# Performance work log

Measured on AMD Instinct MI355X. Metric: run time of the kernel, lower is better.

The kernel has to match this reference:

```python
import jax, jax.numpy as jnp
import numpy as np

N, E, D, L, G = 100000, 800000, 64, 5, 256
ATOM_VOCAB, BOND_VOCAB = 119, 5
BN_EPS = 1e-5

def _bn(h, g, b):
    # BatchNorm1d in training mode: batch mean / biased var over nodes
    m = h.mean(0)
    v = h.var(0)
    return g * (h - m) * jax.lax.rsqrt(v + BN_EPS) + b

def setup_inputs() -> dict:
    key = jax.random.key(0)
    ks = jax.random.split(key, 12)
    xavier = lambda k, fi, fo: jax.random.uniform(k, (fi, fo), jnp.float32,
                                                  -np.sqrt(6.0/(fi+fo)), np.sqrt(6.0/(fi+fo)))
    return {
        "batch": jnp.sort(jax.random.randint(ks[0], (N,), 0, G)),
        "x": jax.random.randint(ks[1], (N, 1), 0, ATOM_VOCAB),
        "edge_index": jax.random.randint(ks[2], (2, E), 0, N),
        "edge_attr": jax.random.randint(ks[3], (E, 1), 0, BOND_VOCAB),
        "atom_emb": jax.random.normal(ks[4], (ATOM_VOCAB, D), jnp.float32),
        "bond_emb": jax.random.normal(ks[5], (BOND_VOCAB, D), jnp.float32),
        "W1": jnp.stack([xavier(jax.random.fold_in(ks[6], i), D, 2*D) for i in range(L)]),
        "b1": jnp.zeros((L, 2*D), jnp.float32),
        "g1": jnp.ones((L, 2*D), jnp.float32),
        "be1": jnp.zeros((L, 2*D), jnp.float32),
        "W2": jnp.stack([xavier(jax.random.fold_in(ks[7], i), 2*D, D) for i in range(L)]),
        "b2": jnp.zeros((L, D), jnp.float32),
        "gbn": jnp.ones((L, D), jnp.float32),
        "bbn": jnp.zeros((L, D), jnp.float32),
    }

def reference(batch, x, edge_index, edge_attr, atom_emb, bond_emb,
              W1, b1, g1, be1, W2, b2, gbn, bbn):
    h = atom_emb[x[:, 0]]              # [N, D]
    ea = bond_emb[edge_attr[:, 0]]     # [E, D]
    src, dst = edge_index[0], edge_index[1]
    for i in range(L):
        msg = jax.nn.relu(h[src] + ea)                         # [E, D]
        aggr = jax.ops.segment_sum(msg, dst, num_segments=N)   # [N, D]
        z = h + aggr                                           # (1+eps)*x_i + aggr, eps=0
        z = _bn(z @ W1[i] + b1[i], g1[i], be1[i])
        z = jax.nn.relu(z) @ W2[i] + b2[i]
        h = _bn(z, gbn[i], bbn[i])                             # outer BN
        if i < L - 1:
            h = jax.nn.relu(h)                                 # drop_ratio = 0 -> no dropout
    xpool = jax.ops.segment_sum(h, batch, num_segments=G)      # global_add_pool
    return (xpool, h)
```

## Files before the change

kernel.cpp:

```cpp
#include <hip/hip_runtime.h>
#include <cstdint>
#include <cstddef>

#define NN 100000
#define NP 100032
#define NE 800000
#define NG 256
#define NL 5
#define EPS 1e-5f
#define NSTRIPE 32

typedef __bf16 bf16x8 __attribute__((ext_vector_type(8)));
typedef float f32x4 __attribute__((ext_vector_type(4)));

__device__ __forceinline__ float bf2f(unsigned short u) {
  union { unsigned int i; float f; } x; x.i = ((unsigned int)u) << 16; return x.f;
}
__device__ __forceinline__ unsigned short f2bf(float f) {
  union { float f; unsigned int i; } x; x.f = f;
  unsigned int r = x.i + 0x7fffu + ((x.i >> 16) & 1u);
  return (unsigned short)(r >> 16);
}

__global__ __launch_bounds__(256) void prep_k(const int* __restrict__ x,
                                              const float* __restrict__ atom_emb,
                                              unsigned short* __restrict__ A,
                                              const float* __restrict__ W1,
                                              const float* __restrict__ W2,
                                              unsigned short* __restrict__ Wt1,
                                              unsigned short* __restrict__ Wt2,
                                              int* __restrict__ cnt) {
  int b = blockIdx.x, t = threadIdx.x;
  if (b < 3125) {
    int i = b * 256 + t;
    int n = i >> 3, c0 = (i & 7) * 8;
    const float* p = atom_emb + (size_t)x[n] * 64 + c0;
    float4 v0 = *(const float4*)p;
    float4 v1 = *(const float4*)(p + 4);
    union { bf16x8 b8; unsigned short u[8]; } o;
    o.u[0] = f2bf(v0.x); o.u[1] = f2bf(v0.y); o.u[2] = f2bf(v0.z); o.u[3] = f2bf(v0.w);
    o.u[4] = f2bf(v1.x); o.u[5] = f2bf(v1.y); o.u[6] = f2bf(v1.z); o.u[7] = f2bf(v1.w);
    *(bf16x8*)(A + (size_t)n * 64 + c0) = o.b8;
  } else if (b < 3445) {
    int i = (b - 3125) * 256 + t;
    const int S = NL * 128 * 64;
    if (i < S) {
      int l = i / (128 * 64), r = i % (128 * 64);
      int c = r / 64, k = r % 64;
      Wt1[i] = f2bf(W1[(size_t)l * 64 * 128 + (size_t)k * 128 + c]);
    } else {
      int j = i - S;
      int l = j / (128 * 64), r = j % (128 * 64);
      int c = r / 128, k = r % 128;
      Wt2[j] = f2bf(W2[(size_t)l * 128 * 64 + (size_t)k * 64 + c]);
    }
  } else {
    int i = (b - 3445) * 256 + t;
    if (i < NN) cnt[i] = 0;
  }
}

__global__ __launch_bounds__(256) void hist_k(const int* __restrict__ ei,
                                              int* __restrict__ cnt) {
  int e = blockIdx.x * 256 + threadIdx.x;
  if (e >= NE) return;
  atomicAdd(&cnt[ei[NE + e]], 1);
}

__global__ __launch_bounds__(256) void scan1_k(const int* __restrict__ cnt,
                                               int* __restrict__ rs,
                                               int* __restrict__ bsum) {
  __shared__ int sh[256];
  int t = threadIdx.x;
  int base = blockIdx.x * 1024 + t * 4;
  int v0 = 0, v1 = 0, v2 = 0, v3 = 0;
  if (base + 0 < NN) v0 = cnt[base + 0];
  if (base + 1 < NN) v1 = cnt[base + 1];
  if (base + 2 < NN) v2 = cnt[base + 2];
  if (base + 3 < NN) v3 = cnt[base + 3];
  int tsum = v0 + v1 + v2 + v3;
  sh[t] = tsum;
  __syncthreads();
  for (int off = 1; off < 256; off <<= 1) {
    int x = (t >= off) ? sh[t - off] : 0;
    __syncthreads();
    sh[t] += x;
    __syncthreads();
  }
  int excl = sh[t] - tsum;
  if (base + 0 < NN) rs[base + 0] = excl;
  if (base + 1 < NN) rs[base + 1] = excl + v0;
  if (base + 2 < NN) rs[base + 2] = excl + v0 + v1;
  if (base + 3 < NN) rs[base + 3] = excl + v0 + v1 + v2;
  if (t == 255) bsum[blockIdx.x] = sh[255];
}

__global__ __launch_bounds__(256) void scan3_k(int* __restrict__ rs,
                                               const int* __restrict__ bsum,
                                               int* __restrict__ cursor) {
  int i = blockIdx.x * 256 + threadIdx.x;
  int chunk = blockIdx.x >> 2;
  int boff = 0;
  for (int j = 0; j < chunk; ++j) boff += bsum[j];
  if (i < NN) {
    int v = rs[i] + boff;
    rs[i] = v;
    cursor[i] = v;
  }
  if (i == 0) rs[NN] = NE;
}

__global__ __launch_bounds__(256) void scatter_k(const int* __restrict__ ei,
                                                 const int* __restrict__ eattr,
                                                 int* __restrict__ cursor,
                                                 int* __restrict__ epack) {
  int band = blockIdx.x & 3;
  int e = (blockIdx.x >> 2) * 256 + threadIdx.x;
  if (e >= NE) return;
  int d = ei[NE + e];
  if (d / 25000 != band) return;
  int slot = atomicAdd(&cursor[d], 1);
  epack[slot] = (ei[e] << 3) | eattr[e];
}

template <int MODE>
__global__ __launch_bounds__(256) void csr_aggr_k(const int* __restrict__ rowstart,
                                                  const int* __restrict__ epack,
                                                  const float* __restrict__ bond,
                                                  const unsigned short* __restrict__ A,
                                                  const float* __restrict__ stat2prev,
                                                  const float* __restrict__ g,
                                                  const float* __restrict__ be,
                                                  const unsigned short* __restrict__ Wt1,
                                                  unsigned short* __restrict__ B,
                                                  float* __restrict__ stat1) {
  __shared__ float bl[5][68];
  __shared__ float scl64[64], shf64[64];
  __shared__ unsigned short Bs[32][72];
  int tid = threadIdx.x;
  for (int j = tid; j < 320; j += 256) bl[j >> 6][j & 63] = bond[j];
  if (MODE && tid < 64) {
    float s = 0.f, s2 = 0.f;
#pragma unroll
    for (int r = 0; r < NSTRIPE; ++r) {
      s += stat2prev[r * 128 + tid];
      s2 += stat2prev[r * 128 + 64 + tid];
    }
    float mean = s * (1.f / NN);
    float var = fmaxf(s2 * (1.f / NN) - mean * mean, 0.f);
    float sc = g[tid] * rsqrtf(var + EPS);
    scl64[tid] = sc;
    shf64[tid] = be[tid] - mean * sc;
  }
  __syncthreads();

  int lane = tid & 63;
  int sg = lane >> 3, ch = lane & 7, c0 = ch * 8;
  int rloc = (tid >> 6) * 8 + sg;
  int row = blockIdx.x * 32 + rloc;
  float sc[8], sf[8];
  if (MODE) {
#pragma unroll
    for (int j = 0; j < 8; ++j) { sc[j] = scl64[c0 + j]; sf[j] = shf64[c0 + j]; }
  }
  int s = rowstart[row], e = rowstart[row + 1];
  float acc[8];
#pragma unroll
  for (int j = 0; j < 8; ++j) acc[j] = 0.f;
  int i = s;
  for (; i + 4 <= e; i += 4) {
    int p0 = epack[i], p1 = epack[i + 1], p2 = epack[i + 2], p3 = epack[i + 3];
    union { bf16x8 b; unsigned short u[8]; } h0, h1, h2, h3;
    h0.b = *(const bf16x8*)(A + (size_t)(p0 >> 3) * 64 + c0);
    h1.b = *(const bf16x8*)(A + (size_t)(p1 >> 3) * 64 + c0);
    h2.b = *(const bf16x8*)(A + (size_t)(p2 >> 3) * 64 + c0);
    h3.b = *(const bf16x8*)(A + (size_t)(p3 >> 3) * 64 + c0);
    const float* bp0 = &bl[p0 & 7][c0];
    const float* bp1 = &bl[p1 & 7][c0];
    const float* bp2 = &bl[p2 & 7][c0];
    const float* bp3 = &bl[p3 & 7][c0];
    float4 x0 = *(const float4*)(bp0), x1 = *(const float4*)(bp0 + 4);
    float4 y0 = *(const float4*)(bp1), y1 = *(const float4*)(bp1 + 4);
    float4 z0 = *(const float4*)(bp2), z1 = *(const float4*)(bp2 + 4);
    float4 w0 = *(const float4*)(bp3), w1 = *(const float4*)(bp3 + 4);
    float b0[8] = {x0.x, x0.y, x0.z, x0.w, x1.x, x1.y, x1.z, x1.w};
    float b1[8] = {y0.x, y0.y, y0.z, y0.w, y1.x, y1.y, y1.z, y1.w};
    float b2v[8] = {z0.x, z0.y, z0.z, z0.w, z1.x, z1.y, z1.z, z1.w};
    float b3[8] = {w0.x, w0.y, w0.z, w0.w, w1.x, w1.y, w1.z, w1.w};
#pragma unroll
    for (int j = 0; j < 8; ++j) {
      float v0 = bf2f(h0.u[j]);
      float v1 = bf2f(h1.u[j]);
      float v2 = bf2f(h2.u[j]);
      float v3 = bf2f(h3.u[j]);
      if (MODE) {
        v0 = fmaxf(fmaf(v0, sc[j], sf[j]), 0.f);
        v1 = fmaxf(fmaf(v1, sc[j], sf[j]), 0.f);
        v2 = fmaxf(fmaf(v2, sc[j], sf[j]), 0.f);
        v3 = fmaxf(fmaf(v3, sc[j], sf[j]), 0.f);
      }
      acc[j] += fmaxf(v0 + b0[j], 0.f);
      acc[j] += fmaxf(v1 + b1[j], 0.f);
      acc[j] += fmaxf(v2 + b2v[j], 0.f);
      acc[j] += fmaxf(v3 + b3[j], 0.f);
    }
  }
  for (; i < e; ++i) {
    int p0 = epack[i];
    union { bf16x8 b; unsigned short u[8]; } h0;
    h0.b = *(const bf16x8*)(A + (size_t)(p0 >> 3) * 64 + c0);
    const float* bp0 = &bl[p0 & 7][c0];
    float4 x0 = *(const float4*)(bp0), x1 = *(const float4*)(bp0 + 4);
    float b0[8] = {x0.x, x0.y, x0.z, x0.w, x1.x, x1.y, x1.z, x1.w};
#pragma unroll
    for (int j = 0; j < 8; ++j) {
      float v0 = bf2f(h0.u[j]);
      if (MODE) v0 = fmaxf(fmaf(v0, sc[j], sf[j]), 0.f);
      acc[j] += fmaxf(v0 + b0[j], 0.f);
    }
  }
  union { bf16x8 b; unsigned short u[8]; } rv, o;
  rv.b = *(const bf16x8*)(A + (size_t)row * 64 + c0);
#pragma unroll
  for (int j = 0; j < 8; ++j) {
    float r = bf2f(rv.u[j]);
    if (MODE) r = fmaxf(fmaf(r, sc[j], sf[j]), 0.f);
    o.u[j] = f2bf(acc[j] + r);
  }
  *(bf16x8*)(B + (size_t)row * 64 + c0) = o.b;
  *(bf16x8*)&Bs[rloc][c0] = o.b;
  __syncthreads();

  int w = tid >> 6;
  int rlo = lane & 15, khi = lane >> 4;
  int tile = w >> 1, gcol = (w & 1) * 64;
  bf16x8 fa0 = *(const bf16x8*)&Bs[tile * 16 + rlo][khi * 8];
  bf16x8 fa1 = *(const bf16x8*)&Bs[tile * 16 + rlo][khi * 8 + 32];
  float* dst = stat1 + (blockIdx.x & (NSTRIPE - 1)) * 256;
#pragma unroll
  for (int ct = 0; ct < 4; ++ct) {
    int c = gcol + ct * 16 + rlo;
    const bf16x8* bp = (const bf16x8*)(Wt1 + (size_t)c * 64 + khi * 8);
    f32x4 yacc;
    yacc[0] = 0.f; yacc[1] = 0.f; yacc[2] = 0.f; yacc[3] = 0.f;
    yacc = __builtin_amdgcn_mfma_f32_16x16x32_bf16(fa0, bp[0], yacc, 0, 0, 0);
    yacc = __builtin_amdgcn_mfma_f32_16x16x32_bf16(fa1, bp[4], yacc, 0, 0, 0);
    float ss = 0.f, ss2 = 0.f;
#pragma unroll
    for (int q = 0; q < 4; ++q) {
      ss += yacc[q];
      ss2 = fmaf(yacc[q], yacc[q], ss2);
    }
    ss += __shfl_xor(ss, 16);  ss += __shfl_xor(ss, 32);
    ss2 += __shfl_xor(ss2, 16); ss2 += __shfl_xor(ss2, 32);
    if (khi == 0) {
      atomicAdd(&dst[c], ss);
      atomicAdd(&dst[128 + c], ss2);
    }
  }
}

__global__ __launch_bounds__(256) void gemm12_k(const unsigned short* __restrict__ B,
                                                const unsigned short* __restrict__ Wt1,
                                                const unsigned short* __restrict__ Wt2,
                                                const float* __restrict__ stat1,
                                                const float* __restrict__ g1,
                                                const float* __restrict__ be1,
                                                const float* __restrict__ b2,
                                                unsigned short* __restrict__ z2b,
                                                float* __restrict__ stat2f) {
  __shared__ unsigned short Zs[64][136];
  __shared__ float sclS[128], shfS[128], sred[128];
  int tid = threadIdx.x;
  int w = tid >> 6, lane = tid & 63;
  int rlo = lane & 15, khi = lane >> 4;
  int row0 = blockIdx.x * 64 + w * 16;
  const bf16x8* ap = (const bf16x8*)(B + (size_t)(row0 + rlo) * 64 + khi * 8);
  bf16x8 a0 = ap[0], a1 = ap[4];
  if (tid < 128) {
    float s = 0.f, s2 = 0.f;
#pragma unroll
    for (int r = 0; r < NSTRIPE; ++r) {
      s += stat1[r * 256 + tid];
      s2 += stat1[r * 256 + 128 + tid];
    }
    float mean = s * (1.f / NN);
    float var = fmaxf(s2 * (1.f / NN) - mean * mean, 0.f);
    float sc = g1[tid] * rsqrtf(var + EPS);
    sclS[tid] = sc;
    shfS[tid] = be1[tid] - mean * sc;
    sred[tid] = 0.f;
  }
  __syncthreads();
#pragma unroll
  for (int ct = 0; ct < 8; ++ct) {
    const bf16x8* bp = (const bf16x8*)(Wt1 + (size_t)(ct * 16 + rlo) * 64 + khi * 8);
    f32x4 acc;
    acc[0] = 0.f; acc[1] = 0.f; acc[2] = 0.f; acc[3] = 0.f;
    acc = __builtin_amdgcn_mfma_f32_16x16x32_bf16(a0, bp[0], acc, 0, 0, 0);
    acc = __builtin_amdgcn_mfma_f32_16x16x32_bf16(a1, bp[4], acc, 0, 0, 0);
    int c = ct * 16 + rlo;
    float sc = sclS[c], sf = shfS[c];
#pragma unroll
    for (int q = 0; q < 4; ++q)
      Zs[w * 16 + khi * 4 + q][c] = f2bf(fmaxf(fmaf(acc[q], sc, sf), 0.f));
  }
  bf16x8 af0 = *(const bf16x8*)&Zs[w * 16 + rlo][khi * 8];
  bf16x8 af1 = *(const bf16x8*)&Zs[w * 16 + rlo][32 + khi * 8];
  bf16x8 af2 = *(const bf16x8*)&Zs[w * 16 + rlo][64 + khi * 8];
  bf16x8 af3 = *(const bf16x8*)&Zs[w * 16 + rlo][96 + khi * 8];
  __syncthreads();
  f32x4 acc2[4];
#pragma unroll
  for (int ct = 0; ct < 4; ++ct) { acc2[ct][0] = 0.f; acc2[ct][1] = 0.f; acc2[ct][2] = 0.f; acc2[ct][3] = 0.f; }
#pragma unroll
  for (int ct = 0; ct < 4; ++ct) {
    const bf16x8* bp = (const bf16x8*)(Wt2 + (size_t)(ct * 16 + rlo) * 128 + khi * 8);
    acc2[ct] = __builtin_amdgcn_mfma_f32_16x16x32_bf16(af0, bp[0], acc2[ct], 0, 0, 0);
    acc2[ct] = __builtin_amdgcn_mfma_f32_16x16x32_bf16(af1, bp[4], acc2[ct], 0, 0, 0);
    acc2[ct] = __builtin_amdgcn_mfma_f32_16x16x32_bf16(af2, bp[8], acc2[ct], 0, 0, 0);
    acc2[ct] = __builtin_amdgcn_mfma_f32_16x16x32_bf16(af3, bp[12], acc2[ct], 0, 0, 0);
  }
  unsigned short (*Z2)[72] = (unsigned short(*)[72])Zs;
#pragma unroll
  for (int ct = 0; ct < 4; ++ct) {
    int c = ct * 16 + rlo;
    float bs = b2[c];
    float s = 0.f, s2 = 0.f;
#pragma unroll
    for (int q = 0; q < 4; ++q) {
      int brow = w * 16 + khi * 4 + q;
      float v = acc2[ct][q] + bs;
      unsigned short ub = f2bf(v);
      Z2[brow][c] = ub;
      float vf = bf2f(ub);
      if (blockIdx.x * 64 + brow < NN) { s += vf; s2 += vf * vf; }
    }
    s += __shfl_xor(s, 16);  s += __shfl_xor(s, 32);
    s2 += __shfl_xor(s2, 16); s2 += __shfl_xor(s2, 32);
    if (khi == 0) {
      atomicAdd(&sred[c], s);
      atomicAdd(&sred[64 + c], s2);
    }
  }
  __syncthreads();
#pragma unroll
  for (int pass = 0; pass < 2; ++pass) {
    int orow = pass * 32 + (tid >> 3), oc0 = (tid & 7) * 8;
    *(bf16x8*)(z2b + (size_t)(blockIdx.x * 64 + orow) * 64 + oc0) =
        *(const bf16x8*)&Z2[orow][oc0];
  }
  if (tid < 128)
    atomicAdd(&stat2f[(blockIdx.x & (NSTRIPE - 1)) * 128 + tid], sred[tid]);
}

__global__ __launch_bounds__(256) void final_k(const unsigned short* __restrict__ A,
                                               const float* __restrict__ stat2f,
                                               const float* __restrict__ g,
                                               const float* __restrict__ be,
                                               const int* __restrict__ batch,
                                               float* __restrict__ hf,
                                               float* __restrict__ xpool) {
  __shared__ float scl[64], shf[64];
  __shared__ float red[16][64];
  __shared__ int gfirst, gsame;
  int tid = threadIdx.x;
  if (tid < 64) {
    float s = 0.f, s2 = 0.f;
#pragma unroll
    for (int r = 0; r < NSTRIPE; ++r) {
      s += stat2f[r * 128 + tid];
      s2 += stat2f[r * 128 + 64 + tid];
    }
    float mean = s * (1.f / NN);
    float var = fmaxf(s2 * (1.f / NN) - mean * mean, 0.f);
    float sc = g[tid] * rsqrtf(var + EPS);
    scl[tid] = sc;
    shf[tid] = be[tid] - mean * sc;
  }
  int n0 = blockIdx.x * 16;
  if (tid == 0) {
    gfirst = batch[n0];
    gsame = (batch[n0] == batch[n0 + 15]) ? 1 : 0;
  }
  __syncthreads();
  int r = tid >> 4, c4 = tid & 15;
  int n = n0 + r;
  ushort4 raw = *(const ushort4*)(A + (size_t)n * 64 + c4 * 4);
  int cb = c4 * 4;
  float4 v;
  v.x = fmaf(bf2f(raw.x), scl[cb + 0], shf[cb + 0]);
  v.y = fmaf(bf2f(raw.y), scl[cb + 1], shf[cb + 1]);
  v.z = fmaf(bf2f(raw.z), scl[cb + 2], shf[cb + 2]);
  v.w = fmaf(bf2f(raw.w), scl[cb + 3], shf[cb + 3]);
  *(float4*)(hf + (size_t)n * 64 + cb) = v;
  *(float4*)&red[r][cb] = v;
  __syncthreads();
  if (gsame) {
#pragma unroll
    for (int off = 8; off >= 1; off >>= 1) {
      if (r < off) {
        float4 a = *(float4*)&red[r][cb];
        float4 b = *(float4*)&red[r + off][cb];
        *(float4*)&red[r][cb] = make_float4(a.x + b.x, a.y + b.y, a.z + b.z, a.w + b.w);
      }
      __syncthreads();
    }
    if (r == 0) {
      float* p = xpool + (size_t)gfirst * 64 + cb;
      float4 a = *(float4*)&red[0][cb];
      atomicAdd(p + 0, a.x); atomicAdd(p + 1, a.y);
      atomicAdd(p + 2, a.z); atomicAdd(p + 3, a.w);
    }
  } else {
    int gg = batch[n];
    float* p = xpool + (size_t)gg * 64 + cb;
    atomicAdd(p + 0, v.x); atomicAdd(p + 1, v.y);
    atomicAdd(p + 2, v.z); atomicAdd(p + 3, v.w);
  }
}

extern "C" void kernel_launch(void* const* d_in, const int* in_sizes, int n_in,
                              void* d_out, int out_size, void* d_ws, size_t ws_size,
                              hipStream_t stream) {
  const int* batch = (const int*)d_in[0];
  const int* x = (const int*)d_in[1];
  const int* ei = (const int*)d_in[2];
  const int* eattr = (const int*)d_in[3];
  const float* atom_emb = (const float*)d_in[4];
  const float* bond_emb = (const float*)d_in[5];
  const float* W1 = (const float*)d_in[6];
  const float* g1 = (const float*)d_in[8];
  const float* be1 = (const float*)d_in[9];
  const float* W2 = (const float*)d_in[10];
  const float* b2 = (const float*)d_in[11];
  const float* gbn = (const float*)d_in[12];
  const float* bbn = (const float*)d_in[13];

  float* out = (float*)d_out;
  float* xpool = out;
  float* hf = out + NG * 64;

  char* ws = (char*)d_ws;
  unsigned short* A   = (unsigned short*)(ws);
  unsigned short* B   = (unsigned short*)(ws + 12804096);
  float* sbuf         = (float*)(ws + 25608192);
  unsigned short* Wt1 = (unsigned short*)(ws + 25853952);
  unsigned short* Wt2 = (unsigned short*)(ws + 25935872);
  int* rowstart       = (int*)(ws + 26017792);
  int* epack          = (int*)(ws + 26417796);
  int* cnt    = (int*)(ws + 12804096);
  int* cursor = (int*)(ws + 12804096 + 1048576);
  int* bsum   = (int*)(ws + 12804096 + 2097152);

  prep_k<<<3836, 256, 0, stream>>>(x, atom_emb, A, W1, W2, Wt1, Wt2, cnt);

  hist_k<<<(NE + 255) / 256, 256, 0, stream>>>(ei, cnt);
  scan1_k<<<98, 256, 0, stream>>>(cnt, rowstart, bsum);
  scan3_k<<<(NN + 255) / 256, 256, 0, stream>>>(rowstart, bsum, cursor);
  scatter_k<<<4 * ((NE + 255) / 256), 256, 0, stream>>>(ei, eattr, cursor, epack);

  hipMemsetAsync(sbuf, 0, 245760, stream);
  for (int l = 0; l < NL; ++l) {
    float* stat1 = sbuf + (size_t)l * 12288;
    float* stat2 = sbuf + (size_t)l * 12288 + 8192;
    float* stat2p = sbuf + (size_t)(l - 1) * 12288 + 8192;
    if (l == 0)
      csr_aggr_k<0><<<NN / 32, 256, 0, stream>>>(rowstart, epack, bond_emb, A,
                                                 sbuf, gbn, bbn,
                                                 Wt1, B, stat1);
    else
      csr_aggr_k<1><<<NN / 32, 256, 0, stream>>>(rowstart, epack, bond_emb, A,
                                                 stat2p, gbn + (size_t)(l - 1) * 64,
                                                 bbn + (size_t)(l - 1) * 64,
                                                 Wt1 + (size_t)l * 128 * 64, B, stat1);
    gemm12_k<<<NP / 64, 256, 0, stream>>>(B, Wt1 + (size_t)l * 128 * 64,
                                          Wt2 + (size_t)l * 64 * 128,
                                          stat1, g1 + (size_t)l * 128, be1 + (size_t)l * 128,
                                          b2 + (size_t)l * 64, A, stat2);
  }

  hipMemsetAsync(xpool, 0, (size_t)NG * 64 * 4, stream);
  final_k<<<NN / 16, 256, 0, stream>>>(A, sbuf + (size_t)(NL - 1) * 12288 + 8192,
                                       gbn + (size_t)(NL - 1) * 64,
                                       bbn + (size_t)(NL - 1) * 64, batch, hf, xpool);
}
```

Baseline: 497.7 us.

## Sort nodes by in-degree so aggregation warps get balanced edge counts

Builds a degree histogram during the scan, prefix-sums it, and counting-sorts node ids into a permutation by in-degree. The CSR aggregation kernel then processes rows in permuted order, so the 8 rows sharing a wavefront have similar edge counts and lanes idle less. The cost is extra preprocessing passes and atomics, one more kernel launch, and an extra indirection. Neighbouring rows in a block are no longer contiguous, which may hurt locality of writes to B.

```diff
diff --git a/kernel.cpp b/kernel.cpp
--- a/kernel.cpp
+++ b/kernel.cpp
@@ -56,7 +56,7 @@
     }
   } else {
     int i = (b - 3445) * 256 + t;
-    if (i < NN) cnt[i] = 0;
+    if (i < NN + 128) cnt[i] = 0;
   }
 }
 
@@ -69,9 +69,12 @@
 
 __global__ __launch_bounds__(256) void scan1_k(const int* __restrict__ cnt,
                                                int* __restrict__ rs,
-                                               int* __restrict__ bsum) {
+                                               int* __restrict__ bsum,
+                                               int* __restrict__ dhist) {
   __shared__ int sh[256];
+  __shared__ int dh[64];
   int t = threadIdx.x;
+  if (t < 64) dh[t] = 0;
   int base = blockIdx.x * 1024 + t * 4;
   int v0 = 0, v1 = 0, v2 = 0, v3 = 0;
   if (base + 0 < NN) v0 = cnt[base + 0];
@@ -81,6 +84,10 @@
   int tsum = v0 + v1 + v2 + v3;
   sh[t] = tsum;
   __syncthreads();
+  if (base + 0 < NN) atomicAdd(&dh[v0 < 63 ? v0 : 63], 1);
+  if (base + 1 < NN) atomicAdd(&dh[v1 < 63 ? v1 : 63], 1);
+  if (base + 2 < NN) atomicAdd(&dh[v2 < 63 ? v2 : 63], 1);
+  if (base + 3 < NN) atomicAdd(&dh[v3 < 63 ? v3 : 63], 1);
   for (int off = 1; off < 256; off <<= 1) {
     int x = (t >= off) ? sh[t - off] : 0;
     __syncthreads();
@@ -93,11 +100,23 @@
   if (base + 2 < NN) rs[base + 2] = excl + v0 + v1;
   if (base + 3 < NN) rs[base + 3] = excl + v0 + v1 + v2;
   if (t == 255) bsum[blockIdx.x] = sh[255];
+  __syncthreads();
+  if (t < 64 && dh[t]) atomicAdd(&dhist[t], dh[t]);
+}
+
+__global__ void dscan_k(const int* __restrict__ dhist, int* __restrict__ dofs) {
+  if (threadIdx.x == 0 && blockIdx.x == 0) {
+    int run = 0;
+    for (int d = 0; d < 64; ++d) { dofs[d] = run; run += dhist[d]; }
+  }
 }
 
 __global__ __launch_bounds__(256) void scan3_k(int* __restrict__ rs,
                                                const int* __restrict__ bsum,
-                                               int* __restrict__ cursor) {
+                                               int* __restrict__ cursor,
+                                               const int* __restrict__ cnt,
+                                               int* __restrict__ dofs,
+                                               int* __restrict__ perm) {
   int i = blockIdx.x * 256 + threadIdx.x;
   int chunk = blockIdx.x >> 2;
   int boff = 0;
@@ -106,6 +125,9 @@
     int v = rs[i] + boff;
     rs[i] = v;
     cursor[i] = v;
+    int d = cnt[i]; if (d > 63) d = 63;
+    int slot = atomicAdd(&dofs[d], 1);
+    perm[slot] = i;
   }
   if (i == 0) rs[NN] = NE;
 }
@@ -132,6 +154,7 @@
                                                   const float* __restrict__ g,
                                                   const float* __restrict__ be,
                                                   const unsigned short* __restrict__ Wt1,
+                                                  const int* __restrict__ perm,
                                                   unsigned short* __restrict__ B,
                                                   float* __restrict__ stat1) {
   __shared__ float bl[5][68];
@@ -157,7 +180,7 @@
   int lane = tid & 63;
   int sg = lane >> 3, ch = lane & 7, c0 = ch * 8;
   int rloc = (tid >> 6) * 8 + sg;
-  int row = blockIdx.x * 32 + rloc;
+  int row = perm[blockIdx.x * 32 + rloc];
   float sc[8], sf[8];
   if (MODE) {
 #pragma unroll
@@ -449,15 +472,19 @@
   unsigned short* Wt2 = (unsigned short*)(ws + 25935872);
   int* rowstart       = (int*)(ws + 26017792);
   int* epack          = (int*)(ws + 26417796);
+  int* perm           = (int*)(ws + 29617800);
   int* cnt    = (int*)(ws + 12804096);
+  int* dhist  = cnt + NN;
+  int* dofs   = cnt + NN + 64;
   int* cursor = (int*)(ws + 12804096 + 1048576);
   int* bsum   = (int*)(ws + 12804096 + 2097152);
 
-  prep_k<<<3836, 256, 0, stream>>>(x, atom_emb, A, W1, W2, Wt1, Wt2, cnt);
+  prep_k<<<3837, 256, 0, stream>>>(x, atom_emb, A, W1, W2, Wt1, Wt2, cnt);
 
   hist_k<<<(NE + 255) / 256, 256, 0, stream>>>(ei, cnt);
-  scan1_k<<<98, 256, 0, stream>>>(cnt, rowstart, bsum);
-  scan3_k<<<(NN + 255) / 256, 256, 0, stream>>>(rowstart, bsum, cursor);
+  scan1_k<<<98, 256, 0, stream>>>(cnt, rowstart, bsum, dhist);
+  dscan_k<<<1, 64, 0, stream>>>(dhist, dofs);
+  scan3_k<<<(NN + 255) / 256, 256, 0, stream>>>(rowstart, bsum, cursor, cnt, dofs, perm);
   scatter_k<<<4 * ((NE + 255) / 256), 256, 0, stream>>>(ei, eattr, cursor, epack);
 
   hipMemsetAsync(sbuf, 0, 245760, stream);
@@ -468,12 +495,12 @@
     if (l == 0)
       csr_aggr_k<0><<<NN / 32, 256, 0, stream>>>(rowstart, epack, bond_emb, A,
                                                  sbuf, gbn, bbn,
-                                                 Wt1, B, stat1);
+                                                 Wt1, perm, B, stat1);
     else
       csr_aggr_k<1><<<NN / 32, 256, 0, stream>>>(rowstart, epack, bond_emb, A,
                                                  stat2p, gbn + (size_t)(l - 1) * 64,
                                                  bbn + (size_t)(l - 1) * 64,
-                                                 Wt1 + (size_t)l * 128 * 64, B, stat1);
+                                                 Wt1 + (size_t)l * 128 * 64, perm, B, stat1);
     gemm12_k<<<NP / 64, 256, 0, stream>>>(B, Wt1 + (size_t)l * 128 * 64,
                                           Wt2 + (size_t)l * 64 * 128,
                                           stat1, g1 + (size_t)l * 128, be1 + (size_t)l * 128,
```

After: 822.1 us. +65.2%, slower.
